# Kernel tuning notes

Measured on AMD Instinct MI355X. Metric: run time of the kernel, lower is better.

Reference implementation:

```python
import jax, jax.numpy as jnp
import numpy as np
from jax import lax

G = 8  # number of RBF grid points (FastKAN default style)
GRID = jnp.linspace(-2.0, 2.0, G)
DENOM = 4.0 / (G - 1)  # grid spacing used as gaussian width


def _fastkan_conv(x, ln_w, ln_b, Wb, bb, Ws):
    # x: [B, C, H, W]; 3x3 conv, stride 1, pad 1 via patch unfold + FastKAN linear
    B, C, H, W = x.shape
    p = lax.conv_general_dilated_patches(x, (3, 3), (1, 1), ((1, 1), (1, 1)))  # [B, C*9, H, W]
    p = p.transpose(0, 2, 3, 1).reshape(B * H * W, C * 9)  # [N, in]
    # LayerNorm over patch features (FastKAN normalizes before the RBF basis)
    mu = p.mean(-1, keepdims=True)
    var = p.var(-1, keepdims=True)
    pn = (p - mu) / jnp.sqrt(var + 1e-5) * ln_w + ln_b
    # Gaussian RBF basis: [N, in, G]
    rbf = jnp.exp(-jnp.square((pn[:, :, None] - GRID) / DENOM))
    spline = rbf.reshape(B * H * W, -1) @ Ws.T          # [N, out]
    base = jax.nn.silu(p) @ Wb.T + bb                    # [N, out]
    out = spline + base
    return out.reshape(B, H, W, -1).transpose(0, 3, 1, 2)  # [B, out, H, W]


def _bn_relu_pool(h, gamma, beta):
    # BatchNorm2d in training mode (batch stats), ReLU, MaxPool2d(2,2)
    mu = h.mean((0, 2, 3), keepdims=True)
    var = h.var((0, 2, 3), keepdims=True)
    h = (h - mu) / jnp.sqrt(var + 1e-5) * gamma[None, :, None, None] + beta[None, :, None, None]
    h = jax.nn.relu(h)
    return lax.reduce_window(h, -jnp.inf, lax.max, (1, 1, 2, 2), (1, 1, 2, 2), 'VALID')


def setup_inputs() -> dict:
    key = jax.random.key(0)
    ks = jax.random.split(key, 16)
    B, Cin, H, W = 32, 16, 64, 64
    dims = [(Cin * 9, 64), (64 * 9, 128), (128 * 9, 256)]
    inp = {"x": jax.random.normal(ks[0], (B, Cin, H, W), jnp.float32)}
    for i, (fin, fout) in enumerate(dims, 1):
        inp[f"ln_w{i}"] = jnp.ones((fin,), jnp.float32)
        inp[f"ln_b{i}"] = jnp.zeros((fin,), jnp.float32)
        inp[f"Wb{i}"] = jax.random.normal(ks[3 * i], (fout, fin), jnp.float32) * 0.05
        inp[f"bb{i}"] = jnp.zeros((fout,), jnp.float32)
        inp[f"Ws{i}"] = jax.random.normal(ks[3 * i + 1], (fout, fin * G), jnp.float32) * 0.05
        inp[f"g{i}"] = jnp.ones((fout,), jnp.float32)
        inp[f"be{i}"] = jnp.zeros((fout,), jnp.float32)
    return inp


def reference(x, ln_w1, ln_b1, Wb1, bb1, Ws1, g1, be1,
              ln_w2, ln_b2, Wb2, bb2, Ws2, g2, be2,
              ln_w3, ln_b3, Wb3, bb3, Ws3, g3, be3):
    h = _bn_relu_pool(_fastkan_conv(x, ln_w1, ln_b1, Wb1, bb1, Ws1), g1, be1)
    h = _bn_relu_pool(_fastkan_conv(h, ln_w2, ln_b2, Wb2, bb2, Ws2), g2, be2)
    h = _bn_relu_pool(_fastkan_conv(h, ln_w3, ln_b3, Wb3, bb3, Ws3), g3, be3)
    return h.reshape(h.shape[0], -1)  # flatten: [B, 256*8*8]
```

## Files before the change

### kernel.cpp

```cpp
#include <hip/hip_runtime.h>

typedef _Float16 half_t;
typedef __attribute__((ext_vector_type(8))) _Float16 half8;
typedef __attribute__((ext_vector_type(4))) float floatx4;


#define RBF_SCALE 2.1019644f
#define RBF_G0   -4.2039288f
#define RBF_2D    2.40224482f
#define RBF_D2    1.44269504f
#define RBF_Q     0.13533528f

template<int C, int H, int W>
__global__ __launch_bounds__(256)
void ln_prep(const float* __restrict__ x,
             const float* __restrict__ lnw, const float* __restrict__ lnb,
             half_t* __restrict__ pn, half_t* __restrict__ sp)
{
    const int HW = H * W, IN = C * 9;
    const int NL = (IN + 63) / 64;
    const int wv = threadIdx.x >> 6, lane = threadIdx.x & 63;
    const int pix = blockIdx.x * 4 + wv;
    const int b = pix / HW, hw = pix % HW, h = hw / W, w = hw % W;
    const float* xb = x + (long)b * C * HW;

    float v[NL];
    float s = 0.f, s2 = 0.f;
    #pragma unroll
    for (int t = 0; t < NL; ++t) {
        int i = t * 64 + lane;
        float val = 0.f;
        if (i < IN) {
            int ch = i / 9, r = i - ch * 9;
            int y = h + r / 3 - 1, xx = w + r % 3 - 1;
            if (y >= 0 && y < H && xx >= 0 && xx < W)
                val = xb[ch * HW + y * W + xx];
        }
        v[t] = val; s += val; s2 += val * val;
    }
    #pragma unroll
    for (int off = 32; off > 0; off >>= 1) {
        s  += __shfl_down(s,  off, 64);
        s2 += __shfl_down(s2, off, 64);
    }
    s = __shfl(s, 0, 64); s2 = __shfl(s2, 0, 64);
    float mean = s / IN;
    float istd = rsqrtf(s2 / IN - mean * mean + 1e-5f);

    #pragma unroll
    for (int t = 0; t < NL; ++t) {
        int i = t * 64 + lane;
        if (i < IN) {
            float val = v[t];
            float pnv = (val - mean) * istd * lnw[i] + lnb[i];
            pnv = fminf(12.f, fmaxf(-12.f, pnv * RBF_SCALE));
            pn[(long)pix * IN + i] = (half_t)pnv;
            sp[(long)pix * IN + i] = (half_t)(val / (1.f + __expf(-val)));
        }
    }
}

template<int IN, int OUT>
__global__ __launch_bounds__(256)
void conv_w(const float* __restrict__ Ws, const float* __restrict__ Wb,
            half_t* __restrict__ Wt)
{
    const int NIB = (IN + 63) / 64, NSTEP = NIB * 9;
    int idx = blockIdx.x * 256 + threadIdx.x;
    if (idx >= OUT * NSTEP * 64) return;
    int uu = idx & 63;
    int t = idx >> 6;
    int o = t % OUT;
    int s = t / OUT;
    int iblk = s / 9, j = s % 9;
    int ulin = (((uu >> 3) ^ (o & 7)) << 3) + (uu & 7);
    int i = iblk * 64 + ulin;
    float v = 0.f;
    if (i < IN)
        v = (j < 8) ? Ws[(long)o * IN * 8 + i * 8 + j] : Wb[(long)o * IN + i];
    Wt[idx] = (half_t)v;
}

template<int IN, int OUT, int HW, int NB, int SPLIT>
__global__ __launch_bounds__(256)
void kan_gemm(const half_t* __restrict__ pn, const half_t* __restrict__ sp,
              const half_t* __restrict__ Wt, float* __restrict__ out)
{
    const int NIB = (IN + 63) / 64;

    __shared__ half_t As[64 * 64];
    __shared__ half_t Bs[NB * 64 * 64];

    const int tid = threadIdx.x;
    const int row = tid >> 2, q = tid & 3;
    const int pix = blockIdx.x * 64 + row;
    const half_t* pnrow = pn + (long)pix * IN;
    const half_t* sprow = sp + (long)pix * IN;

    const int wv = tid >> 6, lane = tid & 63;
    const int lr = lane & 15, lq = lane >> 4;
    const int u0 = (2 * q) ^ (row & 7);
    const int u1 = (2 * q + 1) ^ (row & 7);
    const int yoff = blockIdx.y * (4 * NB * 16);

    floatx4 acc[NB][4] = {};
    float r[16], u[16];
    half8 pf0, pf1;

    const int grpA = (blockIdx.z * NIB) / SPLIT;
    const int grpB = ((blockIdx.z + 1) * NIB) / SPLIT;
    const int s0 = grpA * 9, s1 = grpB * 9;

    int jg = 0, ibg = grpA;

    auto ldglob = [&](const half_t* base, int ib, half8& a, half8& b) {
        int i0 = ib * 64 + q * 16;
        const half_t* pp = base + ((i0 < IN) ? i0 : 0);
        a = *(const half8*)pp;
        b = *(const half8*)(pp + 8);
    };

    auto stageB = [&](int it) {
        const half_t* wsrc = Wt + (long)it * OUT * 64
                              + (long)(yoff + wv * NB * 16) * 64;
        #pragma unroll
        for (int c = 0; c < NB * 2; ++c) {
            __builtin_amdgcn_global_load_lds(
                (const __attribute__((address_space(1))) void*)(wsrc + c * 512 + lane * 8),
                (__attribute__((address_space(3))) void*)(&Bs[wv * NB * 1024 + c * 512]),
                16, 0, 0);
        }
    };

    auto genA = [&]() {
        if (jg < 8) {
            if (jg == 0) {
                #pragma unroll
                for (int kk = 0; kk < 8; ++kk) {
                    float d0 = (float)pf0[kk] - RBF_G0;
                    float d1 = (float)pf1[kk] - RBF_G0;
                    r[kk]     = __builtin_amdgcn_exp2f(-(d0 * d0));
                    u[kk]     = __builtin_amdgcn_exp2f(fmaf(RBF_2D, d0, -RBF_D2));
                    r[kk + 8] = __builtin_amdgcn_exp2f(-(d1 * d1));
                    u[kk + 8] = __builtin_amdgcn_exp2f(fmaf(RBF_2D, d1, -RBF_D2));
                }
            }
            half8 a0, a1;
            #pragma unroll
            for (int kk = 0; kk < 8; ++kk) {
                a0[kk] = (half_t)r[kk];
                a1[kk] = (half_t)r[kk + 8];
            }
            *(half8*)&As[row * 64 + u0 * 8] = a0;
            *(half8*)&As[row * 64 + u1 * 8] = a1;
            if (jg < 7) {
                #pragma unroll
                for (int kk = 0; kk < 16; ++kk) { r[kk] *= u[kk]; u[kk] *= RBF_Q; }
            }
            if (jg == 7) ldglob(sprow, ibg, pf0, pf1);
        } else {
            *(half8*)&As[row * 64 + u0 * 8] = pf0;
            *(half8*)&As[row * 64 + u1 * 8] = pf1;
            ldglob(pnrow, ibg + 1, pf0, pf1);
        }
        if (++jg == 9) { jg = 0; ++ibg; }
    };

    auto domfma = [&]() {
        __builtin_amdgcn_s_setprio(1);
        #pragma unroll
        for (int ks = 0; ks < 2; ++ks) {
            half8 af[4], bf[NB];
            #pragma unroll
            for (int mf = 0; mf < 4; ++mf) {
                int rr = mf * 16 + lr;
                af[mf] = *(const half8*)&As[rr * 64 + (((ks * 4 + lq) ^ (rr & 7)) * 8)];
            }
            #pragma unroll
            for (int nb = 0; nb < NB; ++nb) {
                int rr = wv * NB * 16 + nb * 16 + lr;
                bf[nb] = *(const half8*)&Bs[rr * 64 + (((ks * 4 + lq) ^ (rr & 7)) * 8)];
            }
            #pragma unroll
            for (int nb = 0; nb < NB; ++nb)
                #pragma unroll
                for (int mf = 0; mf < 4; ++mf)
                    acc[nb][mf] = __builtin_amdgcn_mfma_f32_16x16x32_f16(
                        bf[nb], af[mf], acc[nb][mf], 0, 0, 0);
        }
        __builtin_amdgcn_s_setprio(0);
    };

    ldglob(pnrow, grpA, pf0, pf1);

    for (int it = s0; it < s1; ++it) {
        __syncthreads();
        stageB(it);
        genA();
        __syncthreads();
        domfma();
    }

    const long zoff = (long)blockIdx.z * ((long)gridDim.x * 64) * OUT;
    #pragma unroll
    for (int nb = 0; nb < NB; ++nb)
    #pragma unroll
    for (int mf = 0; mf < 4; ++mf)
    #pragma unroll
    for (int reg = 0; reg < 4; ++reg) {
        int o  = yoff + wv * NB * 16 + nb * 16 + lq * 4 + reg;
        int p2 = blockIdx.x * 64 + mf * 16 + lr;
        int b2 = p2 / HW, hw2 = p2 % HW;
        out[zoff + ((long)b2 * OUT + o) * HW + hw2] = acc[nb][mf][reg];
    }
}

__launch_bounds__(256)
__global__ void bn_stats(const float* __restrict__ h, const float* __restrict__ bias,
                         int C, int HW, int B, int nz, float* __restrict__ sums)
{
    int c = blockIdx.y;
    float bbc = bias[c];
    long zstride = (long)B * C * HW;
    int total = B * HW;
    float s = 0.f, s2 = 0.f;
    for (int idx = blockIdx.x * 256 + threadIdx.x; idx < total; idx += 256 * gridDim.x) {
        int b = idx / HW, r = idx % HW;
        long base = ((long)b * C + c) * HW + r;
        float v = bbc;
        for (int z = 0; z < nz; ++z) v += h[z * zstride + base];
        s += v; s2 += v * v;
    }
    for (int off = 32; off > 0; off >>= 1) {
        s  += __shfl_down(s,  off, 64);
        s2 += __shfl_down(s2, off, 64);
    }
    __shared__ float rs[4], rs2[4];
    int lane = threadIdx.x & 63, wid = threadIdx.x >> 6;
    if (lane == 0) { rs[wid] = s; rs2[wid] = s2; }
    __syncthreads();
    if (threadIdx.x == 0) {
        atomicAdd(&sums[c],     rs[0] + rs[1] + rs[2] + rs[3]);
        atomicAdd(&sums[C + c], rs2[0] + rs2[1] + rs2[2] + rs2[3]);
    }
}

__launch_bounds__(256)
__global__ void bn_relu_pool(const float* __restrict__ h, const float* __restrict__ sums,
                             const float* __restrict__ bias,
                             const float* __restrict__ gamma, const float* __restrict__ beta,
                             float* __restrict__ out, int B, int C, int H, int W, int nz)
{
    int Ho = H / 2, Wo = W / 2;
    long total = (long)B * C * Ho * Wo;
    long idx = (long)blockIdx.x * 256 + threadIdx.x;
    if (idx >= total) return;
    int pw = idx % Wo; long t = idx / Wo;
    int ph = t % Ho; t /= Ho;
    int c = t % C; int b = (int)(t / C);

    float M = (float)B * H * W;
    float mean = sums[c] / M;
    float var  = sums[C + c] / M - mean * mean;
    float scale = gamma[c] * rsqrtf(var + 1e-5f);
    float shift = beta[c] - mean * scale + bias[c] * scale;

    long zstride = (long)B * C * H * W;
    const float* hp = h + ((long)b * C + c) * H * W;
    float m = 0.f;
    #pragma unroll
    for (int i = 0; i < 2; ++i)
        #pragma unroll
        for (int j = 0; j < 2; ++j) {
            long off = (2 * ph + i) * W + 2 * pw + j;
            float v = 0.f;
            for (int z = 0; z < nz; ++z) v += hp[z * zstride + off];
            v = v * scale + shift;
            m = fmaxf(m, v);
        }
    out[idx] = m;
}

extern "C" void kernel_launch(void* const* d_in, const int* in_sizes, int n_in,
                              void* d_out, int out_size, void* d_ws, size_t ws_size,
                              hipStream_t stream) {
    const float* x     = (const float*)d_in[0];
    const float* ln_w1 = (const float*)d_in[1];  const float* ln_b1 = (const float*)d_in[2];
    const float* Wb1   = (const float*)d_in[3];  const float* bb1   = (const float*)d_in[4];
    const float* Ws1   = (const float*)d_in[5];  const float* g1    = (const float*)d_in[6];
    const float* be1   = (const float*)d_in[7];
    const float* ln_w2 = (const float*)d_in[8];  const float* ln_b2 = (const float*)d_in[9];
    const float* Wb2   = (const float*)d_in[10]; const float* bb2   = (const float*)d_in[11];
    const float* Ws2   = (const float*)d_in[12]; const float* g2    = (const float*)d_in[13];
    const float* be2   = (const float*)d_in[14];
    const float* ln_w3 = (const float*)d_in[15]; const float* ln_b3 = (const float*)d_in[16];
    const float* Wb3   = (const float*)d_in[17]; const float* bb3   = (const float*)d_in[18];
    const float* Ws3   = (const float*)d_in[19]; const float* g3    = (const float*)d_in[20];
    const float* be3   = (const float*)d_in[21];

    const int B = 32;
    char* ws = (char*)d_ws;
    float*  convbuf = (float*)(ws + 0);
    float*  poolbuf = (float*)(ws + 33554432);
    float*  stats1  = (float*)(ws + 41943040);
    float*  stats2  = (float*)(ws + 41945088);
    float*  stats3  = (float*)(ws + 41947136);
    half_t* wt1     = (half_t*)(ws + 41949184);
    half_t* wt2     = (half_t*)(ws + 42170368);
    half_t* wt3     = (half_t*)(ws + 43497472);
    half_t* pnbuf   = (half_t*)(ws + 48805888);
    half_t* spbuf   = (half_t*)(ws + 86554624);

    hipMemsetAsync(stats1, 0, 6144, stream);

    conv_w<144, 64><<<(64 * 27 * 64 + 255) / 256, 256, 0, stream>>>(Ws1, Wb1, wt1);
    conv_w<576, 128><<<(128 * 81 * 64 + 255) / 256, 256, 0, stream>>>(Ws2, Wb2, wt2);
    conv_w<1152, 256><<<(256 * 162 * 64 + 255) / 256, 256, 0, stream>>>(Ws3, Wb3, wt3);

    {
        const int H = 64, W = 64, OUT = 64;
        int npix = B * H * W;
        ln_prep<16, H, W><<<npix / 4, 256, 0, stream>>>(x, ln_w1, ln_b1, pnbuf, spbuf);
        kan_gemm<144, OUT, H * W, 1, 1><<<dim3(npix / 64, 1, 1), 256, 0, stream>>>(
            pnbuf, spbuf, wt1, convbuf);
        bn_stats<<<dim3(64, OUT), 256, 0, stream>>>(convbuf, bb1, OUT, H * W, B, 1, stats1);
        long tot = (long)B * OUT * (H / 2) * (W / 2);
        bn_relu_pool<<<(tot + 255) / 256, 256, 0, stream>>>(
            convbuf, stats1, bb1, g1, be1, poolbuf, B, OUT, H, W, 1);
    }
    {
        const int H = 32, W = 32, OUT = 128;
        int npix = B * H * W;
        ln_prep<64, H, W><<<npix / 4, 256, 0, stream>>>(poolbuf, ln_w2, ln_b2, pnbuf, spbuf);
        kan_gemm<576, OUT, H * W, 2, 2><<<dim3(npix / 64, 1, 2), 256, 0, stream>>>(
            pnbuf, spbuf, wt2, convbuf);
        bn_stats<<<dim3(16, OUT), 256, 0, stream>>>(convbuf, bb2, OUT, H * W, B, 2, stats2);
        long tot = (long)B * OUT * (H / 2) * (W / 2);
        bn_relu_pool<<<(tot + 255) / 256, 256, 0, stream>>>(
            convbuf, stats2, bb2, g2, be2, poolbuf, B, OUT, H, W, 2);
    }
    {
        const int H = 16, W = 16, OUT = 256;
        int npix = B * H * W;
        ln_prep<128, H, W><<<npix / 4, 256, 0, stream>>>(poolbuf, ln_w3, ln_b3, pnbuf, spbuf);
        kan_gemm<1152, OUT, H * W, 2, 4><<<dim3(npix / 64, 2, 4), 256, 0, stream>>>(
            pnbuf, spbuf, wt3, convbuf);
        bn_stats<<<dim3(8, OUT), 256, 0, stream>>>(convbuf, bb3, OUT, H * W, B, 4, stats3);
        long tot = (long)B * OUT * (H / 2) * (W / 2);
        bn_relu_pool<<<(tot + 255) / 256, 256, 0, stream>>>(
            convbuf, stats3, bb3, g3, be3, (float*)d_out, B, OUT, H, W, 4);
    }
}
```

Measured before the change: 479.5 us.

## Fuse patch unfold, LayerNorm and SiLU into the KAN GEMM A-tile generation

Drops the ln_prep kernel that wrote normalized and SiLU half-precision patch matrices to global memory. A small chan_ss kernel now computes per-pixel channel sum and sum-of-squares. The GEMM derives each patch's LayerNorm stats from the 3x3 neighbourhood of these sums, then gathers raw input values, normalizes them and computes the RBF and SiLU terms inline. This removes a large 9x-expanded intermediate write and read, at the cost of scattered gathers and extra ALU work inside the GEMM main loop, repeated across the y and z split blocks.

```diff
diff --git a/kernel.cpp b/kernel.cpp
--- a/kernel.cpp
+++ b/kernel.cpp
@@ -10,54 +10,22 @@
 #define RBF_2D    2.40224482f
 #define RBF_D2    1.44269504f
 #define RBF_Q     0.13533528f
-
-template<int C, int H, int W>
+#define LOG2E     1.44269504f
+
+template<int C, int HW>
 __global__ __launch_bounds__(256)
-void ln_prep(const float* __restrict__ x,
-             const float* __restrict__ lnw, const float* __restrict__ lnb,
-             half_t* __restrict__ pn, half_t* __restrict__ sp)
-{
-    const int HW = H * W, IN = C * 9;
-    const int NL = (IN + 63) / 64;
-    const int wv = threadIdx.x >> 6, lane = threadIdx.x & 63;
-    const int pix = blockIdx.x * 4 + wv;
-    const int b = pix / HW, hw = pix % HW, h = hw / W, w = hw % W;
-    const float* xb = x + (long)b * C * HW;
-
-    float v[NL];
+void chan_ss(const float* __restrict__ src, float2* __restrict__ ss)
+{
+    int idx = blockIdx.x * 256 + threadIdx.x;
+    int b = idx / HW, hw = idx - b * HW;
+    const float* p = src + (long)b * C * HW + hw;
     float s = 0.f, s2 = 0.f;
-    #pragma unroll
-    for (int t = 0; t < NL; ++t) {
-        int i = t * 64 + lane;
-        float val = 0.f;
-        if (i < IN) {
-            int ch = i / 9, r = i - ch * 9;
-            int y = h + r / 3 - 1, xx = w + r % 3 - 1;
-            if (y >= 0 && y < H && xx >= 0 && xx < W)
-                val = xb[ch * HW + y * W + xx];
-        }
-        v[t] = val; s += val; s2 += val * val;
-    }
-    #pragma unroll
-    for (int off = 32; off > 0; off >>= 1) {
-        s  += __shfl_down(s,  off, 64);
-        s2 += __shfl_down(s2, off, 64);
-    }
-    s = __shfl(s, 0, 64); s2 = __shfl(s2, 0, 64);
-    float mean = s / IN;
-    float istd = rsqrtf(s2 / IN - mean * mean + 1e-5f);
-
-    #pragma unroll
-    for (int t = 0; t < NL; ++t) {
-        int i = t * 64 + lane;
-        if (i < IN) {
-            float val = v[t];
-            float pnv = (val - mean) * istd * lnw[i] + lnb[i];
-            pnv = fminf(12.f, fmaxf(-12.f, pnv * RBF_SCALE));
-            pn[(long)pix * IN + i] = (half_t)pnv;
-            sp[(long)pix * IN + i] = (half_t)(val / (1.f + __expf(-val)));
-        }
-    }
+    #pragma unroll 4
+    for (int c = 0; c < C; ++c) {
+        float v = p[(long)c * HW];
+        s += v; s2 += v * v;
+    }
+    ss[idx] = make_float2(s, s2);
 }
 
 template<int IN, int OUT>
@@ -81,11 +49,13 @@
     Wt[idx] = (half_t)v;
 }
 
-template<int IN, int OUT, int HW, int NB, int SPLIT>
+template<int C, int OUT, int H, int W, int NB, int SPLIT>
 __global__ __launch_bounds__(256)
-void kan_gemm(const half_t* __restrict__ pn, const half_t* __restrict__ sp,
+void kan_gemm(const float* __restrict__ src, const float2* __restrict__ ss,
+              const float* __restrict__ lnw, const float* __restrict__ lnb,
               const half_t* __restrict__ Wt, float* __restrict__ out)
 {
+    const int IN = C * 9, HW = H * W;
     const int NIB = (IN + 63) / 64;
 
     __shared__ half_t As[64 * 64];
@@ -94,8 +64,9 @@
     const int tid = threadIdx.x;
     const int row = tid >> 2, q = tid & 3;
     const int pix = blockIdx.x * 64 + row;
-    const half_t* pnrow = pn + (long)pix * IN;
-    const half_t* sprow = sp + (long)pix * IN;
+    const int bb = pix / HW, hw = pix - bb * HW;
+    const int h = hw / W, w = hw - h * W;
+    const float* srcb = src + (long)bb * C * HW;
 
     const int wv = tid >> 6, lane = tid & 63;
     const int lr = lane & 15, lq = lane >> 4;
@@ -103,22 +74,31 @@
     const int u1 = (2 * q + 1) ^ (row & 7);
     const int yoff = blockIdx.y * (4 * NB * 16);
 
+    float mean, istd;
+    {
+        float s = 0.f, s2 = 0.f;
+        #pragma unroll
+        for (int dy = -1; dy <= 1; ++dy)
+            #pragma unroll
+            for (int dx = -1; dx <= 1; ++dx) {
+                int y = h + dy, xx = w + dx;
+                if (y >= 0 && y < H && xx >= 0 && xx < W) {
+                    float2 v = ss[(long)bb * HW + y * W + xx];
+                    s += v.x; s2 += v.y;
+                }
+            }
+        mean = s / IN;
+        istd = rsqrtf(s2 / IN - mean * mean + 1e-5f);
+    }
+
     floatx4 acc[NB][4] = {};
-    float r[16], u[16];
-    half8 pf0, pf1;
+    float r[16], u[16], xv[16];
 
     const int grpA = (blockIdx.z * NIB) / SPLIT;
     const int grpB = ((blockIdx.z + 1) * NIB) / SPLIT;
     const int s0 = grpA * 9, s1 = grpB * 9;
 
     int jg = 0, ibg = grpA;
-
-    auto ldglob = [&](const half_t* base, int ib, half8& a, half8& b) {
-        int i0 = ib * 64 + q * 16;
-        const half_t* pp = base + ((i0 < IN) ? i0 : 0);
-        a = *(const half8*)pp;
-        b = *(const half8*)(pp + 8);
-    };
 
     auto stageB = [&](int it) {
         const half_t* wsrc = Wt + (long)it * OUT * 64
@@ -133,36 +113,47 @@
     };
 
     auto genA = [&]() {
+        if (jg == 0) {
+            const int i0 = ibg * 64 + q * 16;
+            #pragma unroll
+            for (int kk = 0; kk < 16; ++kk) {
+                int i = i0 + kk;
+                int ch = i / 9, rr = i - ch * 9;
+                int dy = rr / 3, dx = rr - dy * 3;
+                int y = h + dy - 1, xx = w + dx - 1;
+                bool inb = (ch < C) && (y >= 0) && (y < H) && (xx >= 0) && (xx < W);
+                float xval = inb ? srcb[(long)ch * HW + y * W + xx] : 0.f;
+                xv[kk] = xval;
+                float lw = (i < IN) ? lnw[i] : 0.f;
+                float lb = (i < IN) ? lnb[i] : 0.f;
+                float pnv = (xval - mean) * istd * lw + lb;
+                pnv = fminf(12.f, fmaxf(-12.f, pnv * RBF_SCALE));
+                float d = pnv - RBF_G0;
+                r[kk] = __builtin_amdgcn_exp2f(-(d * d));
+                u[kk] = __builtin_amdgcn_exp2f(fmaf(RBF_2D, d, -RBF_D2));
+            }
+        }
+        half8 a0, a1;
         if (jg < 8) {
-            if (jg == 0) {
-                #pragma unroll
-                for (int kk = 0; kk < 8; ++kk) {
-                    float d0 = (float)pf0[kk] - RBF_G0;
-                    float d1 = (float)pf1[kk] - RBF_G0;
-                    r[kk]     = __builtin_amdgcn_exp2f(-(d0 * d0));
-                    u[kk]     = __builtin_amdgcn_exp2f(fmaf(RBF_2D, d0, -RBF_D2));
-                    r[kk + 8] = __builtin_amdgcn_exp2f(-(d1 * d1));
-                    u[kk + 8] = __builtin_amdgcn_exp2f(fmaf(RBF_2D, d1, -RBF_D2));
-                }
-            }
-            half8 a0, a1;
             #pragma unroll
             for (int kk = 0; kk < 8; ++kk) {
                 a0[kk] = (half_t)r[kk];
                 a1[kk] = (half_t)r[kk + 8];
             }
-            *(half8*)&As[row * 64 + u0 * 8] = a0;
-            *(half8*)&As[row * 64 + u1 * 8] = a1;
             if (jg < 7) {
                 #pragma unroll
                 for (int kk = 0; kk < 16; ++kk) { r[kk] *= u[kk]; u[kk] *= RBF_Q; }
             }
-            if (jg == 7) ldglob(sprow, ibg, pf0, pf1);
         } else {
-            *(half8*)&As[row * 64 + u0 * 8] = pf0;
-            *(half8*)&As[row * 64 + u1 * 8] = pf1;
-            ldglob(pnrow, ibg + 1, pf0, pf1);
-        }
+            #pragma unroll
+            for (int kk = 0; kk < 8; ++kk) {
+                float x0 = xv[kk], x1 = xv[kk + 8];
+                a0[kk] = (half_t)(x0 / (1.f + __builtin_amdgcn_exp2f(-x0 * LOG2E)));
+                a1[kk] = (half_t)(x1 / (1.f + __builtin_amdgcn_exp2f(-x1 * LOG2E)));
+            }
+        }
+        *(half8*)&As[row * 64 + u0 * 8] = a0;
+        *(half8*)&As[row * 64 + u1 * 8] = a1;
         if (++jg == 9) { jg = 0; ++ibg; }
     };
 
@@ -190,8 +181,6 @@
         }
         __builtin_amdgcn_s_setprio(0);
     };
-
-    ldglob(pnrow, grpA, pf0, pf1);
 
     for (int it = s0; it < s1; ++it) {
         __syncthreads();
@@ -308,8 +297,7 @@
     half_t* wt1     = (half_t*)(ws + 41949184);
     half_t* wt2     = (half_t*)(ws + 42170368);
     half_t* wt3     = (half_t*)(ws + 43497472);
-    half_t* pnbuf   = (half_t*)(ws + 48805888);
-    half_t* spbuf   = (half_t*)(ws + 86554624);
+    float2* ssbuf   = (float2*)(ws + 48805888);
 
     hipMemsetAsync(stats1, 0, 6144, stream);
 
@@ -320,9 +308,9 @@
     {
         const int H = 64, W = 64, OUT = 64;
         int npix = B * H * W;
-        ln_prep<16, H, W><<<npix / 4, 256, 0, stream>>>(x, ln_w1, ln_b1, pnbuf, spbuf);
-        kan_gemm<144, OUT, H * W, 1, 1><<<dim3(npix / 64, 1, 1), 256, 0, stream>>>(
-            pnbuf, spbuf, wt1, convbuf);
+        chan_ss<16, H * W><<<npix / 256, 256, 0, stream>>>(x, ssbuf);
+        kan_gemm<16, OUT, H, W, 1, 1><<<dim3(npix / 64, 1, 1), 256, 0, stream>>>(
+            x, ssbuf, ln_w1, ln_b1, wt1, convbuf);
         bn_stats<<<dim3(64, OUT), 256, 0, stream>>>(convbuf, bb1, OUT, H * W, B, 1, stats1);
         long tot = (long)B * OUT * (H / 2) * (W / 2);
         bn_relu_pool<<<(tot + 255) / 256, 256, 0, stream>>>(
@@ -331,9 +319,9 @@
     {
         const int H = 32, W = 32, OUT = 128;
         int npix = B * H * W;
-        ln_prep<64, H, W><<<npix / 4, 256, 0, stream>>>(poolbuf, ln_w2, ln_b2, pnbuf, spbuf);
-        kan_gemm<576, OUT, H * W, 2, 2><<<dim3(npix / 64, 1, 2), 256, 0, stream>>>(
-            pnbuf, spbuf, wt2, convbuf);
+        chan_ss<64, H * W><<<npix / 256, 256, 0, stream>>>(poolbuf, ssbuf);
+        kan_gemm<64, OUT, H, W, 2, 2><<<dim3(npix / 64, 1, 2), 256, 0, stream>>>(
+            poolbuf, ssbuf, ln_w2, ln_b2, wt2, convbuf);
         bn_stats<<<dim3(16, OUT), 256, 0, stream>>>(convbuf, bb2, OUT, H * W, B, 2, stats2);
         long tot = (long)B * OUT * (H / 2) * (W / 2);
         bn_relu_pool<<<(tot + 255) / 256, 256, 0, stream>>>(
@@ -342,9 +330,9 @@
     {
         const int H = 16, W = 16, OUT = 256;
         int npix = B * H * W;
-        ln_prep<128, H, W><<<npix / 4, 256, 0, stream>>>(poolbuf, ln_w3, ln_b3, pnbuf, spbuf);
-        kan_gemm<1152, OUT, H * W, 2, 4><<<dim3(npix / 64, 2, 4), 256, 0, stream>>>(
-            pnbuf, spbuf, wt3, convbuf);
+        chan_ss<128, H * W><<<npix / 256, 256, 0, stream>>>(poolbuf, ssbuf);
+        kan_gemm<128, OUT, H, W, 2, 4><<<dim3(npix / 64, 2, 4), 256, 0, stream>>>(
+            poolbuf, ssbuf, ln_w3, ln_b3, wt3, convbuf);
         bn_stats<<<dim3(8, OUT), 256, 0, stream>>>(convbuf, bb3, OUT, H * W, B, 4, stats3);
         long tot = (long)B * OUT * (H / 2) * (W / 2);
         bn_relu_pool<<<(tot + 255) / 256, 256, 0, stream>>>(
```

Result: slower. 504.9 us (+5.3%).
